# Performance work log

Measured on AMD Instinct MI355X. Metric: run time of the kernel, lower is better.

The kernel has to match this reference:

```python
import jax, jax.numpy as jnp
import numpy as np

TEMPERATURE = 0.1


def setup_inputs() -> dict:
    key = jax.random.key(0)
    k1, k2 = jax.random.split(key)
    N, D = 8192, 128
    features = jax.random.normal(k1, (N, D), dtype=jnp.float32)
    labels = jax.random.randint(k2, (N,), 0, 1000, dtype=jnp.int64)
    return {"features": features, "labels": labels}


def reference(features, labels):
    N = features.shape[0]
    # L2-normalize rows
    feats = features / jnp.linalg.norm(features, axis=1, keepdims=True)
    # positive-pair mask from labels [N, N]
    labels = labels.reshape(-1, 1)
    mask = (labels == labels.T).astype(feats.dtype)
    # similarity matrix scaled by temperature
    sim = jnp.matmul(feats, feats.T) / TEMPERATURE
    # exclude self-comparisons (diagonal)
    logits_mask = 1.0 - jnp.eye(N, dtype=feats.dtype)
    mask = mask * logits_mask
    exp_logits = jnp.exp(sim) * logits_mask
    log_prob = sim - jnp.log(exp_logits.sum(axis=1, keepdims=True) + 1e-9)
    mask_sum = mask.sum(axis=1)
    mask_sum = jnp.where(mask_sum == 0, jnp.ones_like(mask_sum), mask_sum)
    mean_log_prob_pos = (mask * log_prob).sum(axis=1) / mask_sum
    return -mean_log_prob_pos.mean()
```

## Files before the change

### kernel.cpp

```cpp
#include <hip/hip_runtime.h>
#include <hip/hip_bf16.h>
#include <math.h>


constexpr int N = 8192;
constexpr int D = 128;

typedef __attribute__((ext_vector_type(8))) short short8;
typedef __attribute__((ext_vector_type(4))) float f32x4;

__device__ __forceinline__ float fast_exp2(float x) {
#if __has_builtin(__builtin_amdgcn_exp2f)
    return __builtin_amdgcn_exp2f(x);
#else
    return __expf(x * 0.69314718056f);
#endif
}

__device__ __forceinline__ void gload_lds16(const void* g, void* s) {
    __builtin_amdgcn_global_load_lds(
        (const __attribute__((address_space(1))) unsigned int*)g,
        (__attribute__((address_space(3))) unsigned int*)s, 16, 0, 0);
}

__global__ void prep_kernel(const float* __restrict__ F,
                            unsigned short* __restrict__ Fb,
                            float* __restrict__ rowExp,
                            float* __restrict__ rowPos,
                            float* __restrict__ rowCnt) {
    int row = blockIdx.x * 4 + (threadIdx.x >> 6);
    int l = threadIdx.x & 63;
    float2 v = ((const float2*)(F + (size_t)row * D))[l];
    float ss = v.x * v.x + v.y * v.y;
#pragma unroll
    for (int off = 32; off > 0; off >>= 1) ss += __shfl_xor(ss, off);
    float sc = sqrtf(14.4269504089f / ss);
    __hip_bfloat16 hx = __float2bfloat16(v.x * sc);
    __hip_bfloat16 hy = __float2bfloat16(v.y * sc);
    ushort2 u;
    u.x = *(unsigned short*)&hx;
    u.y = *(unsigned short*)&hy;
    ((ushort2*)(Fb + (size_t)row * D))[l] = u;
    if (l == 0) {
        rowExp[row] = 0.0f;
        rowPos[row] = 0.0f;
        rowCnt[row] = 0.0f;
    }
}

__device__ __forceinline__ void stage_tile(const unsigned short* __restrict__ src,
                                           unsigned short* dst, int row0,
                                           int w, int lr, int lq) {
#pragma unroll
    for (int it = 0; it < 4; ++it) {
        int rbase = w * 16 + it * 4;
        int r = rbase + lr;
        int q = lq ^ (r & 7);
        gload_lds16(src + ((size_t)(row0 + r) * D + q * 8), dst + rbase * D);
    }
}

template <bool DIAG>
__device__ __forceinline__ void tile_epilogue(
    const f32x4 (&acc)[2][4], const int (&li)[2][4], const int* lj,
    int wy, int wx, int quad, int c,
    float (&RE)[2][4], float (&RP)[2][4], float (&RC)[2][4]) {
#pragma unroll
    for (int m = 0; m < 2; ++m) {
#pragma unroll
        for (int n = 0; n < 4; ++n) {
#pragma unroll
            for (int r = 0; r < 4; ++r) {
                float s2 = acc[m][n][r];
                bool self = DIAG && ((wy * 32 + m * 16 + quad * 4 + r) ==
                                     (wx * 64 + n * 16 + c));
                bool pos = (li[m][r] == lj[n]) && !self;
                RE[m][r] += self ? 0.0f : fast_exp2(s2);
                RP[m][r] += pos ? s2 : 0.0f;
                RC[m][r] += pos ? 1.0f : 0.0f;
            }
        }
    }
}

__global__ __launch_bounds__(512, 4) void sim_kernel(
    const unsigned short* __restrict__ Fb, const int* __restrict__ labels,
    float* __restrict__ rowExp, float* __restrict__ rowPos,
    float* __restrict__ rowCnt) {
    __shared__ unsigned short At[128 * D];
    __shared__ unsigned short Bt[128 * D];

    const int ti = blockIdx.y;
    const int tjs = blockIdx.x * 8;
    const int i0 = ti * 128;

    const int t = threadIdx.x, w = t >> 6, l = t & 63;
    const int lr = l >> 4, lq = l & 15;
    const int c = l & 15, quad = l >> 4;
    const int wy = w & 3, wx = w >> 2;

    stage_tile(Fb, At, i0, w, lr, lq);
    stage_tile(Fb, Bt, tjs * 128, w, lr, lq);

    int li[2][4];
#pragma unroll
    for (int m = 0; m < 2; ++m)
#pragma unroll
        for (int r = 0; r < 4; ++r)
            li[m][r] = labels[i0 + wy * 32 + m * 16 + quad * 4 + r];

    float RE[2][4] = {}, RP[2][4] = {}, RC[2][4] = {};

    for (int s = 0; s < 8; ++s) {
        int tj = tjs + s, j0 = tj * 128;
        int lj[4];
#pragma unroll
        for (int n = 0; n < 4; ++n) lj[n] = labels[j0 + wx * 64 + n * 16 + c];
        __syncthreads();
        f32x4 acc[2][4] = {};
#pragma unroll
        for (int kk = 0; kk < 4; ++kk) {
            int sl = (kk * 4 + quad) ^ (c & 7);
            short8 af[2], bf[4];
#pragma unroll
            for (int m = 0; m < 2; ++m)
                af[m] = *(const short8*)&At[(wy * 32 + m * 16 + c) * D + sl * 8];
#pragma unroll
            for (int n = 0; n < 4; ++n)
                bf[n] = *(const short8*)&Bt[(wx * 64 + n * 16 + c) * D + sl * 8];
#pragma unroll
            for (int m = 0; m < 2; ++m)
#pragma unroll
                for (int n = 0; n < 4; ++n)
                    acc[m][n] = __builtin_amdgcn_mfma_f32_16x16x32_bf16(
                        af[m], bf[n], acc[m][n], 0, 0, 0);
        }
        __syncthreads();
        if (s < 7) stage_tile(Fb, Bt, (tj + 1) * 128, w, lr, lq);

        if (tj == ti)
            tile_epilogue<true>(acc, li, lj, wy, wx, quad, c, RE, RP, RC);
        else
            tile_epilogue<false>(acc, li, lj, wy, wx, quad, c, RE, RP, RC);
    }

#pragma unroll
    for (int m = 0; m < 2; ++m)
#pragma unroll
        for (int r = 0; r < 4; ++r) {
#pragma unroll
            for (int off = 1; off < 16; off <<= 1) {
                RE[m][r] += __shfl_xor(RE[m][r], off);
                RP[m][r] += __shfl_xor(RP[m][r], off);
                RC[m][r] += __shfl_xor(RC[m][r], off);
            }
        }
    if (c == 0) {
#pragma unroll
        for (int m = 0; m < 2; ++m)
#pragma unroll
            for (int r = 0; r < 4; ++r) {
                int gi = i0 + wy * 32 + m * 16 + quad * 4 + r;
                atomicAdd(&rowExp[gi], RE[m][r]);
                atomicAdd(&rowPos[gi], RP[m][r]);
                atomicAdd(&rowCnt[gi], RC[m][r]);
            }
    }
}

__global__ void finalize_kernel(const float* __restrict__ rowExp,
                                const float* __restrict__ rowPos,
                                const float* __restrict__ rowCnt,
                                float* __restrict__ out) {
    int t = threadIdx.x;
    float a = 0.0f;
    for (int i = t; i < N; i += 1024) {
        float cnt = rowCnt[i];
        if (cnt > 0.5f)
            a += __logf(rowExp[i] + 1e-9f) -
                 0.69314718056f * rowPos[i] / cnt;
    }
#pragma unroll
    for (int off = 32; off > 0; off >>= 1) a += __shfl_xor(a, off);
    __shared__ float ws16[16];
    if ((t & 63) == 0) ws16[t >> 6] = a;
    __syncthreads();
    if (t == 0) {
        float s = 0.0f;
#pragma unroll
        for (int i = 0; i < 16; ++i) s += ws16[i];
        out[0] = s / (float)N;
    }
}

extern "C" void kernel_launch(void* const* d_in, const int* in_sizes, int n_in,
                              void* d_out, int out_size, void* d_ws, size_t ws_size,
                              hipStream_t stream) {
    const float* F      = (const float*)d_in[0];
    const int*   labels = (const int*)d_in[1];
    float* out = (float*)d_out;

    unsigned short* Fb = (unsigned short*)d_ws;
    float* rowExp = (float*)(Fb + (size_t)N * D);
    float* rowPos = rowExp + N;
    float* rowCnt = rowPos + N;

    prep_kernel<<<N / 4, 256, 0, stream>>>(F, Fb, rowExp, rowPos, rowCnt);
    sim_kernel<<<dim3(8, 64), 512, 0, stream>>>(Fb, labels, rowExp, rowPos, rowCnt);
    finalize_kernel<<<1, 1024, 0, stream>>>(rowExp, rowPos, rowCnt, out);
}
```

Baseline: 111.4 us.

## Drop LDS staging, read B fragments from global, use partial buffers and label histogram

```diff
diff --git a/kernel.cpp b/kernel.cpp
--- a/kernel.cpp
+++ b/kernel.cpp
@@ -17,18 +17,10 @@
 #endif
 }
 
-__device__ __forceinline__ void gload_lds16(const void* g, void* s) {
-    __builtin_amdgcn_global_load_lds(
-        (const __attribute__((address_space(1))) unsigned int*)g,
-        (__attribute__((address_space(3))) unsigned int*)s, 16, 0, 0);
-}
-
 __global__ void prep_kernel(const float* __restrict__ F,
                             unsigned short* __restrict__ Fb,
-                            float* __restrict__ rowExp,
-                            float* __restrict__ rowPos,
-                            float* __restrict__ rowCnt) {
-    int row = blockIdx.x * 4 + (threadIdx.x >> 6);
+                            float* __restrict__ out) {
+    int row = blockIdx.x * 16 + (threadIdx.x >> 6);
     int l = threadIdx.x & 63;
     float2 v = ((const float2*)(F + (size_t)row * D))[l];
     float ss = v.x * v.x + v.y * v.y;
@@ -41,155 +33,123 @@
     u.x = *(unsigned short*)&hx;
     u.y = *(unsigned short*)&hy;
     ((ushort2*)(Fb + (size_t)row * D))[l] = u;
-    if (l == 0) {
-        rowExp[row] = 0.0f;
-        rowPos[row] = 0.0f;
-        rowCnt[row] = 0.0f;
-    }
+    if (blockIdx.x == 0 && threadIdx.x == 0) out[0] = 0.0f;
 }
 
-__device__ __forceinline__ void stage_tile(const unsigned short* __restrict__ src,
-                                           unsigned short* dst, int row0,
-                                           int w, int lr, int lq) {
+__global__ __launch_bounds__(256, 4) void sim_kernel(
+    const unsigned short* __restrict__ Fb, const int* __restrict__ labels,
+    float* __restrict__ pE, float* __restrict__ pP) {
+    const int chunk = blockIdx.x;
+    const int by = blockIdx.y;
+    const int i0 = by * 64;
+    const int t = threadIdx.x, w = t >> 6, l = t & 63;
+    const int c = l & 15, quad = l >> 4;
+    const int r0 = i0 + w * 16;
+
+    short8 af[4];
+    const unsigned short* arow = Fb + (size_t)(r0 + c) * D;
 #pragma unroll
-    for (int it = 0; it < 4; ++it) {
-        int rbase = w * 16 + it * 4;
-        int r = rbase + lr;
-        int q = lq ^ (r & 7);
-        gload_lds16(src + ((size_t)(row0 + r) * D + q * 8), dst + rbase * D);
+    for (int kk = 0; kk < 4; ++kk)
+        af[kk] = *(const short8*)(arow + (kk * 4 + quad) * 8);
+
+    int li[4];
+#pragma unroll
+    for (int r = 0; r < 4; ++r) li[r] = labels[r0 + quad * 4 + r];
+
+    float RE[4] = {}, RP[4] = {};
+
+#pragma unroll 2
+    for (int s = 0; s < 16; ++s) {
+        const int jt = chunk * 16 + s;
+        const int j0 = jt * 64;
+        int lj[4];
+#pragma unroll
+        for (int n = 0; n < 4; ++n) lj[n] = labels[j0 + n * 16 + c];
+
+        f32x4 acc[4] = {};
+#pragma unroll
+        for (int kk = 0; kk < 4; ++kk) {
+            short8 bf[4];
+#pragma unroll
+            for (int n = 0; n < 4; ++n)
+                bf[n] = *(const short8*)&Fb[(size_t)(j0 + n * 16 + c) * D +
+                                            (kk * 4 + quad) * 8];
+#pragma unroll
+            for (int n = 0; n < 4; ++n)
+                acc[n] = __builtin_amdgcn_mfma_f32_16x16x32_bf16(
+                    af[kk], bf[n], acc[n], 0, 0, 0);
+        }
+
+        if (jt == by) {
+#pragma unroll
+            for (int n = 0; n < 4; ++n)
+#pragma unroll
+                for (int r = 0; r < 4; ++r) {
+                    float s2 = acc[n][r];
+                    bool self = (w * 16 + quad * 4 + r) == (n * 16 + c);
+                    bool pos = (li[r] == lj[n]) && !self;
+                    RE[r] += self ? 0.0f : fast_exp2(s2);
+                    RP[r] += pos ? s2 : 0.0f;
+                }
+        } else {
+#pragma unroll
+            for (int n = 0; n < 4; ++n)
+#pragma unroll
+                for (int r = 0; r < 4; ++r) {
+                    float s2 = acc[n][r];
+                    RE[r] += fast_exp2(s2);
+                    RP[r] += (li[r] == lj[n]) ? s2 : 0.0f;
+                }
+        }
     }
-}
 
-template <bool DIAG>
-__device__ __forceinline__ void tile_epilogue(
-    const f32x4 (&acc)[2][4], const int (&li)[2][4], const int* lj,
-    int wy, int wx, int quad, int c,
-    float (&RE)[2][4], float (&RP)[2][4], float (&RC)[2][4]) {
 #pragma unroll
-    for (int m = 0; m < 2; ++m) {
+    for (int r = 0; r < 4; ++r) {
 #pragma unroll
-        for (int n = 0; n < 4; ++n) {
+        for (int off = 1; off < 16; off <<= 1) {
+            RE[r] += __shfl_xor(RE[r], off);
+            RP[r] += __shfl_xor(RP[r], off);
+        }
+    }
+    if (c == 0) {
 #pragma unroll
-            for (int r = 0; r < 4; ++r) {
-                float s2 = acc[m][n][r];
-                bool self = DIAG && ((wy * 32 + m * 16 + quad * 4 + r) ==
-                                     (wx * 64 + n * 16 + c));
-                bool pos = (li[m][r] == lj[n]) && !self;
-                RE[m][r] += self ? 0.0f : fast_exp2(s2);
-                RP[m][r] += pos ? s2 : 0.0f;
-                RC[m][r] += pos ? 1.0f : 0.0f;
-            }
+        for (int r = 0; r < 4; ++r) {
+            int row = r0 + quad * 4 + r;
+            pE[row * 8 + chunk] = RE[r];
+            pP[row * 8 + chunk] = RP[r];
         }
     }
 }
 
-__global__ __launch_bounds__(512, 4) void sim_kernel(
-    const unsigned short* __restrict__ Fb, const int* __restrict__ labels,
-    float* __restrict__ rowExp, float* __restrict__ rowPos,
-    float* __restrict__ rowCnt) {
-    __shared__ unsigned short At[128 * D];
-    __shared__ unsigned short Bt[128 * D];
+__global__ void finalize_kernel(const float* __restrict__ pE,
+                                const float* __restrict__ pP,
+                                const int* __restrict__ labels,
+                                float* __restrict__ out) {
+    __shared__ int h[1024];
+    int t = threadIdx.x;
+#pragma unroll
+    for (int i = 0; i < 4; ++i) h[t + i * 256] = 0;
+    __syncthreads();
+    for (int i = t; i < N; i += 256) atomicAdd(&h[labels[i]], 1);
+    __syncthreads();
 
-    const int ti = blockIdx.y;
-    const int tjs = blockIdx.x * 8;
-    const int i0 = ti * 128;
-
-    const int t = threadIdx.x, w = t >> 6, l = t & 63;
-    const int lr = l >> 4, lq = l & 15;
-    const int c = l & 15, quad = l >> 4;
-    const int wy = w & 3, wx = w >> 2;
-
-    stage_tile(Fb, At, i0, w, lr, lq);
-    stage_tile(Fb, Bt, tjs * 128, w, lr, lq);
-
-    int li[2][4];
+    float a = 0.0f;
+    if (t < 64) {
+        int row = blockIdx.x * 64 + t;
+        int cnt = h[labels[row]] - 1;
+        if (cnt > 0) {
+            const float4* e = (const float4*)(pE + row * 8);
+            const float4* p = (const float4*)(pP + row * 8);
+            float4 e0 = e[0], e1 = e[1], p0 = p[0], p1 = p[1];
+            float E = (e0.x + e0.y) + (e0.z + e0.w) +
+                      (e1.x + e1.y) + (e1.z + e1.w);
+            float P = (p0.x + p0.y) + (p0.z + p0.w) +
+                      (p1.x + p1.y) + (p1.z + p1.w);
+            a = __logf(E + 1e-9f) - 0.69314718056f * P / (float)cnt;
+        }
 #pragma unroll
-    for (int m = 0; m < 2; ++m)
-#pragma unroll
-        for (int r = 0; r < 4; ++r)
-            li[m][r] = labels[i0 + wy * 32 + m * 16 + quad * 4 + r];
-
-    float RE[2][4] = {}, RP[2][4] = {}, RC[2][4] = {};
-
-    for (int s = 0; s < 8; ++s) {
-        int tj = tjs + s, j0 = tj * 128;
-        int lj[4];
-#pragma unroll
-        for (int n = 0; n < 4; ++n) lj[n] = labels[j0 + wx * 64 + n * 16 + c];
-        __syncthreads();
-        f32x4 acc[2][4] = {};
-#pragma unroll
-        for (int kk = 0; kk < 4; ++kk) {
-            int sl = (kk * 4 + quad) ^ (c & 7);
-            short8 af[2], bf[4];
-#pragma unroll
-            for (int m = 0; m < 2; ++m)
-                af[m] = *(const short8*)&At[(wy * 32 + m * 16 + c) * D + sl * 8];
-#pragma unroll
-            for (int n = 0; n < 4; ++n)
-                bf[n] = *(const short8*)&Bt[(wx * 64 + n * 16 + c) * D + sl * 8];
-#pragma unroll
-            for (int m = 0; m < 2; ++m)
-#pragma unroll
-                for (int n = 0; n < 4; ++n)
-                    acc[m][n] = __builtin_amdgcn_mfma_f32_16x16x32_bf16(
-                        af[m], bf[n], acc[m][n], 0, 0, 0);
-        }
-        __syncthreads();
-        if (s < 7) stage_tile(Fb, Bt, (tj + 1) * 128, w, lr, lq);
-
-        if (tj == ti)
-            tile_epilogue<true>(acc, li, lj, wy, wx, quad, c, RE, RP, RC);
-        else
-            tile_epilogue<false>(acc, li, lj, wy, wx, quad, c, RE, RP, RC);
-    }
-
-#pragma unroll
-    for (int m = 0; m < 2; ++m)
-#pragma unroll
-        for (int r = 0; r < 4; ++r) {
-#pragma unroll
-            for (int off = 1; off < 16; off <<= 1) {
-                RE[m][r] += __shfl_xor(RE[m][r], off);
-                RP[m][r] += __shfl_xor(RP[m][r], off);
-                RC[m][r] += __shfl_xor(RC[m][r], off);
-            }
-        }
-    if (c == 0) {
-#pragma unroll
-        for (int m = 0; m < 2; ++m)
-#pragma unroll
-            for (int r = 0; r < 4; ++r) {
-                int gi = i0 + wy * 32 + m * 16 + quad * 4 + r;
-                atomicAdd(&rowExp[gi], RE[m][r]);
-                atomicAdd(&rowPos[gi], RP[m][r]);
-                atomicAdd(&rowCnt[gi], RC[m][r]);
-            }
-    }
-}
-
-__global__ void finalize_kernel(const float* __restrict__ rowExp,
-                                const float* __restrict__ rowPos,
-                                const float* __restrict__ rowCnt,
-                                float* __restrict__ out) {
-    int t = threadIdx.x;
-    float a = 0.0f;
-    for (int i = t; i < N; i += 1024) {
-        float cnt = rowCnt[i];
-        if (cnt > 0.5f)
-            a += __logf(rowExp[i] + 1e-9f) -
-                 0.69314718056f * rowPos[i] / cnt;
-    }
-#pragma unroll
-    for (int off = 32; off > 0; off >>= 1) a += __shfl_xor(a, off);
-    __shared__ float ws16[16];
-    if ((t & 63) == 0) ws16[t >> 6] = a;
-    __syncthreads();
-    if (t == 0) {
-        float s = 0.0f;
-#pragma unroll
-        for (int i = 0; i < 16; ++i) s += ws16[i];
-        out[0] = s / (float)N;
+        for (int off = 32; off > 0; off >>= 1) a += __shfl_xor(a, off);
+        if (t == 0) atomicAdd(out, a * (1.0f / (float)N));
     }
 }
 
@@ -201,11 +161,10 @@
     float* out = (float*)d_out;
 
     unsigned short* Fb = (unsigned short*)d_ws;
-    float* rowExp = (float*)(Fb + (size_t)N * D);
-    float* rowPos = rowExp + N;
-    float* rowCnt = rowPos + N;
+    float* pE = (float*)(Fb + (size_t)N * D);
+    float* pP = pE + (size_t)N * 8;
 
-    prep_kernel<<<N / 4, 256, 0, stream>>>(F, Fb, rowExp, rowPos, rowCnt);
-    sim_kernel<<<dim3(8, 64), 512, 0, stream>>>(Fb, labels, rowExp, rowPos, rowCnt);
-    finalize_kernel<<<1, 1024, 0, stream>>>(rowExp, rowPos, rowCnt, out);
+    prep_kernel<<<N / 16, 1024, 0, stream>>>(F, Fb, out);
+    sim_kernel<<<dim3(8, 128), 256, 0, stream>>>(Fb, labels, pE, pP);
+    finalize_kernel<<<128, 256, 0, stream>>>(pE, pP, labels, out);
 }
```

Result: slower. 183.2 us (+64.4%).
